# Performance work log

Measured on AMD Instinct MI355X. Metric: run time of the kernel, lower is better.

## Reference

```python
import jax, jax.numpy as jnp
import numpy as np

NPOINT = 1024
NSAMPLE = 32
BN_EPS = 1e-5


def setup_inputs() -> dict:
    key = jax.random.key(0)
    ks = jax.random.split(key, 8)
    B, N, C = 16, 4096, 64
    chans = [C + 3, 64, 64, 128]
    d = {
        "xyz": jax.random.normal(ks[0], (B, N, 3), jnp.float32),
        "points": jax.random.normal(ks[1], (B, N, C), jnp.float32),
    }
    for i in range(3):
        d[f"w{i+1}"] = jax.random.normal(ks[2 + i], (chans[i + 1], chans[i]), jnp.float32) / np.sqrt(chans[i]).astype(np.float32)
        d[f"b{i+1}"] = jnp.zeros((chans[i + 1],), jnp.float32)
        d[f"g{i+1}"] = jnp.ones((chans[i + 1],), jnp.float32)
        d[f"be{i+1}"] = jnp.zeros((chans[i + 1],), jnp.float32)
    return d


def farthest_point_sample(xyz, npoint):
    # xyz: [B, N, 3] -> centroids: [B, npoint] int32 (deterministic start at index 0)
    B, N, _ = xyz.shape

    def step(carry, _):
        distance, farthest = carry
        centroid = jnp.take_along_axis(xyz, farthest[:, None, None], axis=1)  # [B,1,3]
        dist = jnp.sum((xyz - centroid) ** 2, axis=-1)                         # [B,N]
        distance = jnp.minimum(distance, dist)
        new_far = jnp.argmax(distance, axis=-1).astype(jnp.int32)
        return (distance, new_far), farthest

    init = (jnp.full((B, N), 1e10, xyz.dtype), jnp.zeros((B,), jnp.int32))
    _, cents = jax.lax.scan(step, init, None, length=npoint)  # [npoint, B]
    return cents.T  # [B, npoint]


def index_points(points, idx):
    # points: [B,N,C], idx: [B,...] -> [B,...,C]
    return jax.vmap(lambda p, i: p[i])(points, idx)


def bn_relu(h, g, be):
    # training-mode BatchNorm over all axes except channel (last), biased var
    m = h.mean(axis=(0, 1, 2), keepdims=True)
    v = h.var(axis=(0, 1, 2), keepdims=True)
    return jax.nn.relu((h - m) / jnp.sqrt(v + BN_EPS) * g + be)


def reference(xyz, points, w1, b1, g1, be1, w2, b2, g2, be2, w3, b3, g3, be3):
    # --- sample_and_group ---
    fps_idx = farthest_point_sample(xyz, NPOINT)           # [B,S]
    new_xyz = index_points(xyz, fps_idx)                   # [B,S,3]
    # query_ball_point in source ignores radius: kNN via argsort of sq dists
    sqrdists = jnp.sum((new_xyz[:, :, None, :] - xyz[:, None, :, :]) ** 2, axis=-1)  # [B,S,N]
    _, group_idx = jax.lax.top_k(-sqrdists, NSAMPLE)       # [B,S,K] smallest distances
    grouped_xyz = index_points(xyz, group_idx) - new_xyz[:, :, None, :]  # [B,S,K,3]
    grouped_pts = index_points(points, group_idx)          # [B,S,K,C]
    new_points = jnp.concatenate([grouped_xyz, grouped_pts], axis=-1)    # [B,S,K,C+3]
    # --- shared MLP (1x1 conv + BN + ReLU) x3, channel-last layout ---
    h = bn_relu(jnp.einsum("bskc,oc->bsko", new_points, w1) + b1, g1, be1)
    h = bn_relu(jnp.einsum("bskc,oc->bsko", h, w2) + b2, g2, be2)
    h = bn_relu(jnp.einsum("bskc,oc->bsko", h, w3) + b3, g3, be3)
    # max-pool over the neighbor (nsample) axis
    out = jnp.max(h, axis=2)  # [B,S,128]
    return (new_xyz, out)
```

## Files before the change

### kernel.cpp

```cpp
#include <hip/hip_runtime.h>
#include <cstdint>

#define NB   16
#define NPT  4096
#define CINP 64
#define SP   1024
#define KNB  32
#define NROWS (NB*SP*KNB)
#define NT_F  524288.0f
#define NBLK  8192

__device__ __forceinline__ float sqdist3(float ax, float ay, float az,
                                         float bx, float by, float bz) {
  float dx = ax - bx, dy = ay - by, dz = az - bz;
  return __fadd_rn(__fadd_rn(__fmul_rn(dx, dx), __fmul_rn(dy, dy)), __fmul_rn(dz, dz));
}

__global__ __launch_bounds__(512) void fps_kernel(const float* __restrict__ xyz,
                                                  float* __restrict__ newxyz) {
  const int b = blockIdx.x, t = threadIdx.x;
  __shared__ float s_xyz[NPT * 3];
  __shared__ unsigned long long s_red[2][8];
  for (int i = t; i < NPT * 3; i += 512) s_xyz[i] = xyz[b * NPT * 3 + i];
  __syncthreads();
  float px[8], py[8], pz[8], dst[8];
#pragma unroll
  for (int j = 0; j < 8; ++j) {
    int p = t + j * 512;
    px[j] = s_xyz[p * 3 + 0];
    py[j] = s_xyz[p * 3 + 1];
    pz[j] = s_xyz[p * 3 + 2];
    dst[j] = 1e10f;
  }
  float cx = s_xyz[0], cy = s_xyz[1], cz = s_xyz[2];
  const int w = t >> 6, lane = t & 63;
  int buf = 0;
  for (int it = 0; it < SP; ++it) {
    if (t == 0) {
      float* o = newxyz + (b * SP + it) * 3;
      o[0] = cx; o[1] = cy; o[2] = cz;
    }
    unsigned long long best = 0;
#pragma unroll
    for (int j = 0; j < 8; ++j) {
      float d = sqdist3(px[j], py[j], pz[j], cx, cy, cz);
      dst[j] = fminf(dst[j], d);
      unsigned long long key =
          ((unsigned long long)__float_as_uint(dst[j]) << 32) |
          (unsigned)(4095 - (t + j * 512));
      best = key > best ? key : best;
    }
#pragma unroll
    for (int off = 32; off >= 1; off >>= 1) {
      unsigned long long o2 = __shfl_down(best, off);
      best = o2 > best ? o2 : best;
    }
    if (lane == 0) s_red[buf][w] = best;
    __syncthreads();
    unsigned long long k = s_red[buf][0];
#pragma unroll
    for (int i = 1; i < 8; ++i) {
      unsigned long long v = s_red[buf][i];
      k = v > k ? v : k;
    }
    int p = 4095 - (int)(k & 0xFFFFFFFFull);
    cx = s_xyz[p * 3 + 0];
    cy = s_xyz[p * 3 + 1];
    cz = s_xyz[p * 3 + 2];
    buf ^= 1;
  }
}

__global__ __launch_bounds__(256) void knn_kernel(const float* __restrict__ xyz,
                                                  const float* __restrict__ newxyz,
                                                  int* __restrict__ gidx) {
  const int t = threadIdx.x, lane = t & 63, w = t >> 6;
  const int q = blockIdx.x * 4 + w;
  const int b = q >> 10;
  const float* nx = newxyz + q * 3;
  const float qx = nx[0], qy = nx[1], qz = nx[2];
  const float* xb = xyz + b * NPT * 3;
  float d[64];
#pragma unroll
  for (int j = 0; j < 64; ++j) {
    int p = j * 64 + lane;
    d[j] = sqdist3(xb[p * 3], xb[p * 3 + 1], xb[p * 3 + 2], qx, qy, qz);
  }
  unsigned V = 0;
  for (int bit = 30; bit >= 0; --bit) {
    unsigned cand = V | (1u << bit);
    int c = 0;
#pragma unroll
    for (int j = 0; j < 64; ++j) c += (__float_as_uint(d[j]) < cand) ? 1 : 0;
#pragma unroll
    for (int off = 32; off >= 1; off >>= 1) c += __shfl_xor(c, off);
    if (c < KNB) V = cand;
  }
  __shared__ int s_cnt[4], s_eqcnt[4], s_eq[4][64];
  if (lane == 0) { s_cnt[w] = 0; s_eqcnt[w] = 0; }
  __syncthreads();
  int* gout = gidx + q * KNB;
#pragma unroll
  for (int j = 0; j < 64; ++j) {
    unsigned db = __float_as_uint(d[j]);
    if (db < V) {
      int pos = atomicAdd(&s_cnt[w], 1);
      if (pos < KNB) gout[pos] = j * 64 + lane;
    } else if (db == V) {
      int pos = atomicAdd(&s_eqcnt[w], 1);
      if (pos < 64) s_eq[w][pos] = j * 64 + lane;
    }
  }
  __syncthreads();
  if (lane == 0) {
    int c1 = s_cnt[w]; if (c1 > KNB) c1 = KNB;
    int ne = s_eqcnt[w]; if (ne > 64) ne = 64;
    int need = KNB - c1;
    for (int m = 0; m < need; ++m) {
      int bi = -1, bv = 0x7fffffff;
      for (int e = 0; e < ne; ++e) {
        int v = s_eq[w][e];
        if (v < bv) { bv = v; bi = e; }
      }
      gout[c1 + m] = bv;
      if (bi >= 0) s_eq[w][bi] = 0x7fffffff;
    }
  }
}

__global__ __launch_bounds__(256) void layer1_kernel(
    const float* __restrict__ xyz, const float* __restrict__ points,
    const float* __restrict__ newxyz, const int* __restrict__ gidx,
    const float* __restrict__ w1, const float* __restrict__ b1,
    float* __restrict__ h1, float* __restrict__ part) {
  const int t = threadIdx.x, blk = blockIdx.x;
  const int R0 = blk * 64;
  const int b = R0 >> 15;
  __shared__ __align__(16) float xs[67][68];
  __shared__ __align__(16) float wsm[67][68];
  __shared__ float red[2][16][64];
  {
    int o = t & 63;
    for (int c = t >> 6; c < 67; c += 4) wsm[c][o] = w1[o * 67 + c];
  }
  {
    int r = t >> 2, q = t & 3;
    int R = R0 + r;
    int idx = gidx[R];
    if (q == 0) {
      const float* xp = xyz + (size_t)(b * NPT + idx) * 3;
      const float* nq = newxyz + (size_t)(R >> 5) * 3;
      xs[0][r] = xp[0] - nq[0];
      xs[1][r] = xp[1] - nq[1];
      xs[2][r] = xp[2] - nq[2];
    }
    const float* pp = points + (size_t)(b * NPT + idx) * CINP + q * 16;
#pragma unroll
    for (int i = 0; i < 4; ++i) {
      float4 v = *(const float4*)(pp + i * 4);
      int c = 3 + q * 16 + i * 4;
      xs[c][r] = v.x; xs[c + 1][r] = v.y; xs[c + 2][r] = v.z; xs[c + 3][r] = v.w;
    }
  }
  __syncthreads();
  const int tr = t & 15, to = t >> 4;
  float acc[4][4];
#pragma unroll
  for (int j = 0; j < 4; ++j) {
    float bb = b1[to * 4 + j];
    acc[0][j] = bb; acc[1][j] = bb; acc[2][j] = bb; acc[3][j] = bb;
  }
  for (int c = 0; c < 67; ++c) {
    float4 xv = *(const float4*)&xs[c][tr * 4];
    float4 wv = *(const float4*)&wsm[c][to * 4];
    float xa[4] = {xv.x, xv.y, xv.z, xv.w};
    float wa[4] = {wv.x, wv.y, wv.z, wv.w};
#pragma unroll
    for (int i = 0; i < 4; ++i)
#pragma unroll
      for (int j = 0; j < 4; ++j) acc[i][j] += xa[i] * wa[j];
  }
#pragma unroll
  for (int i = 0; i < 4; ++i) {
    float4 st; st.x = acc[i][0]; st.y = acc[i][1]; st.z = acc[i][2]; st.w = acc[i][3];
    *(float4*)&h1[(size_t)(R0 + tr * 4 + i) * 64 + to * 4] = st;
  }
#pragma unroll
  for (int j = 0; j < 4; ++j) {
    float s1 = acc[0][j] + acc[1][j] + acc[2][j] + acc[3][j];
    float s2 = acc[0][j] * acc[0][j] + acc[1][j] * acc[1][j] +
               acc[2][j] * acc[2][j] + acc[3][j] * acc[3][j];
    red[0][tr][to * 4 + j] = s1;
    red[1][tr][to * 4 + j] = s2;
  }
  __syncthreads();
  if (t < 128) {
    int stat = t >> 6, o = t & 63;
    float v = 0.f;
#pragma unroll
    for (int k = 0; k < 16; ++k) v += red[stat][k][o];
    part[(size_t)(stat * 64 + o) * NBLK + blk] = v;
  }
}

__global__ __launch_bounds__(256) void layer2_kernel(
    const float* __restrict__ hin, const float* __restrict__ bn,
    const float* __restrict__ w2, const float* __restrict__ b2,
    float* __restrict__ hout, float* __restrict__ part) {
  const int t = threadIdx.x, blk = blockIdx.x;
  const size_t R0 = (size_t)blk * 64;
  __shared__ __align__(16) float xs[64][68];
  __shared__ __align__(16) float wsm[64][68];
  __shared__ float red[2][16][64];
  {
    int o = t & 63;
    for (int c = t >> 6; c < 64; c += 4) wsm[c][o] = w2[o * 64 + c];
  }
  {
    int r = t >> 2, q = t & 3;
    const float* hp = hin + (R0 + r) * 64 + q * 16;
#pragma unroll
    for (int i = 0; i < 4; ++i) {
      int c = q * 16 + i * 4;
      float4 v = *(const float4*)(hp + i * 4);
      float4 sc = *(const float4*)(bn + c);
      float4 sh = *(const float4*)(bn + 64 + c);
      xs[c][r]     = fmaxf(v.x * sc.x + sh.x, 0.f);
      xs[c + 1][r] = fmaxf(v.y * sc.y + sh.y, 0.f);
      xs[c + 2][r] = fmaxf(v.z * sc.z + sh.z, 0.f);
      xs[c + 3][r] = fmaxf(v.w * sc.w + sh.w, 0.f);
    }
  }
  __syncthreads();
  const int tr = t & 15, to = t >> 4;
  float acc[4][4];
#pragma unroll
  for (int j = 0; j < 4; ++j) {
    float bb = b2[to * 4 + j];
    acc[0][j] = bb; acc[1][j] = bb; acc[2][j] = bb; acc[3][j] = bb;
  }
  for (int c = 0; c < 64; ++c) {
    float4 xv = *(const float4*)&xs[c][tr * 4];
    float4 wv = *(const float4*)&wsm[c][to * 4];
    float xa[4] = {xv.x, xv.y, xv.z, xv.w};
    float wa[4] = {wv.x, wv.y, wv.z, wv.w};
#pragma unroll
    for (int i = 0; i < 4; ++i)
#pragma unroll
      for (int j = 0; j < 4; ++j) acc[i][j] += xa[i] * wa[j];
  }
#pragma unroll
  for (int i = 0; i < 4; ++i) {
    float4 st; st.x = acc[i][0]; st.y = acc[i][1]; st.z = acc[i][2]; st.w = acc[i][3];
    *(float4*)&hout[(R0 + tr * 4 + i) * 64 + to * 4] = st;
  }
#pragma unroll
  for (int j = 0; j < 4; ++j) {
    float s1 = acc[0][j] + acc[1][j] + acc[2][j] + acc[3][j];
    float s2 = acc[0][j] * acc[0][j] + acc[1][j] * acc[1][j] +
               acc[2][j] * acc[2][j] + acc[3][j] * acc[3][j];
    red[0][tr][to * 4 + j] = s1;
    red[1][tr][to * 4 + j] = s2;
  }
  __syncthreads();
  if (t < 128) {
    int stat = t >> 6, o = t & 63;
    float v = 0.f;
#pragma unroll
    for (int k = 0; k < 16; ++k) v += red[stat][k][o];
    part[(size_t)(stat * 64 + o) * NBLK + blk] = v;
  }
}

__global__ __launch_bounds__(256) void layer3_kernel(
    const float* __restrict__ hin, const float* __restrict__ bn,
    const float* __restrict__ w3, const float* __restrict__ b3,
    float* __restrict__ maxh, float* __restrict__ minh, float* __restrict__ part) {
  const int t = threadIdx.x, blk = blockIdx.x;
  const size_t R0 = (size_t)blk * 64;
  __shared__ __align__(16) float smem[64 * 68 + 64 * 136];
  float* xs = smem;
  float* wsm = smem + 64 * 68;
  {
    int o = t & 127, q = t >> 7;
    for (int c = q; c < 64; c += 2) wsm[c * 136 + o] = w3[o * 64 + c];
  }
  {
    int r = t >> 2, q = t & 3;
    const float* hp = hin + (R0 + r) * 64 + q * 16;
#pragma unroll
    for (int i = 0; i < 4; ++i) {
      int c = q * 16 + i * 4;
      float4 v = *(const float4*)(hp + i * 4);
      float4 sc = *(const float4*)(bn + c);
      float4 sh = *(const float4*)(bn + 64 + c);
      xs[c * 68 + r]       = fmaxf(v.x * sc.x + sh.x, 0.f);
      xs[(c + 1) * 68 + r] = fmaxf(v.y * sc.y + sh.y, 0.f);
      xs[(c + 2) * 68 + r] = fmaxf(v.z * sc.z + sh.z, 0.f);
      xs[(c + 3) * 68 + r] = fmaxf(v.w * sc.w + sh.w, 0.f);
    }
  }
  __syncthreads();
  const int tr = t & 15, to = t >> 4;
  float acc[4][8];
#pragma unroll
  for (int j = 0; j < 8; ++j) {
    float bb = b3[to * 8 + j];
#pragma unroll
    for (int i = 0; i < 4; ++i) acc[i][j] = bb;
  }
  for (int c = 0; c < 64; ++c) {
    float4 xv = *(const float4*)&xs[c * 68 + tr * 4];
    float4 wv0 = *(const float4*)&wsm[c * 136 + to * 8];
    float4 wv1 = *(const float4*)&wsm[c * 136 + to * 8 + 4];
    float xa[4] = {xv.x, xv.y, xv.z, xv.w};
    float wa[8] = {wv0.x, wv0.y, wv0.z, wv0.w, wv1.x, wv1.y, wv1.z, wv1.w};
#pragma unroll
    for (int i = 0; i < 4; ++i)
#pragma unroll
      for (int j = 0; j < 8; ++j) acc[i][j] += xa[i] * wa[j];
  }
  __syncthreads();
  float* red = smem;
#pragma unroll
  for (int j = 0; j < 8; ++j) {
    float s1 = acc[0][j] + acc[1][j] + acc[2][j] + acc[3][j];
    float s2 = acc[0][j] * acc[0][j] + acc[1][j] * acc[1][j] +
               acc[2][j] * acc[2][j] + acc[3][j] * acc[3][j];
    red[(0 * 16 + tr) * 128 + to * 8 + j] = s1;
    red[(1 * 16 + tr) * 128 + to * 8 + j] = s2;
  }
  __syncthreads();
  {
    int stat = t >> 7, o = t & 127;
    float v = 0.f;
#pragma unroll
    for (int k = 0; k < 16; ++k) v += red[(stat * 16 + k) * 128 + o];
    part[(size_t)(stat * 128 + o) * NBLK + blk] = v;
  }
  __syncthreads();
#pragma unroll
  for (int j = 0; j < 8; ++j) {
    float mx = fmaxf(fmaxf(acc[0][j], acc[1][j]), fmaxf(acc[2][j], acc[3][j]));
    float mn = fminf(fminf(acc[0][j], acc[1][j]), fminf(acc[2][j], acc[3][j]));
    red[(0 * 16 + tr) * 128 + to * 8 + j] = mx;
    red[(1 * 16 + tr) * 128 + to * 8 + j] = mn;
  }
  __syncthreads();
  {
    int g = t >> 7, o = t & 127;
    float mx = -1e30f, mn = 1e30f;
#pragma unroll
    for (int k = 0; k < 8; ++k) {
      mx = fmaxf(mx, red[(0 * 16 + g * 8 + k) * 128 + o]);
      mn = fminf(mn, red[(1 * 16 + g * 8 + k) * 128 + o]);
    }
    size_t bs = (size_t)blk * 2 + g;
    maxh[bs * 128 + o] = mx;
    minh[bs * 128 + o] = mn;
  }
}

__global__ __launch_bounds__(256) void bn_finalize(const float* __restrict__ part,
                                                   const float* __restrict__ g,
                                                   const float* __restrict__ be,
                                                   float* __restrict__ bnout, int Cout) {
  const int o = blockIdx.x, t = threadIdx.x;
  float s1 = 0.f, s2 = 0.f;
  const float* p1 = part + (size_t)o * NBLK;
  const float* p2 = part + (size_t)(Cout + o) * NBLK;
  for (int i = t; i < NBLK; i += 256) { s1 += p1[i]; s2 += p2[i]; }
#pragma unroll
  for (int off = 32; off >= 1; off >>= 1) {
    s1 += __shfl_xor(s1, off);
    s2 += __shfl_xor(s2, off);
  }
  __shared__ float r1[4], r2[4];
  if ((t & 63) == 0) { r1[t >> 6] = s1; r2[t >> 6] = s2; }
  __syncthreads();
  if (t == 0) {
    float S1 = r1[0] + r1[1] + r1[2] + r1[3];
    float S2 = r2[0] + r2[1] + r2[2] + r2[3];
    float m = S1 / NT_F;
    float v = S2 / NT_F - m * m;
    if (v < 0.f) v = 0.f;
    float inv = 1.0f / sqrtf(v + 1e-5f);
    float sc = g[o] * inv;
    bnout[o] = sc;
    bnout[Cout + o] = be[o] - m * sc;
  }
}

__global__ __launch_bounds__(256) void finalize_kernel(const float* __restrict__ maxh,
                                                       const float* __restrict__ minh,
                                                       const float* __restrict__ bn,
                                                       float* __restrict__ out2) {
  int i = blockIdx.x * 256 + threadIdx.x;
  int o = i & 127;
  float sc = bn[o], sh = bn[128 + o];
  float a = sc * maxh[i] + sh;
  float c = sc * minh[i] + sh;
  out2[i] = fmaxf(fmaxf(a, c), 0.f);
}

extern "C" void kernel_launch(void* const* d_in, const int* in_sizes, int n_in,
                              void* d_out, int out_size, void* d_ws, size_t ws_size,
                              hipStream_t stream) {
  const float* xyz = (const float*)d_in[0];
  const float* points = (const float*)d_in[1];
  const float* w1 = (const float*)d_in[2];
  const float* b1 = (const float*)d_in[3];
  const float* g1 = (const float*)d_in[4];
  const float* be1 = (const float*)d_in[5];
  const float* w2 = (const float*)d_in[6];
  const float* b2 = (const float*)d_in[7];
  const float* g2 = (const float*)d_in[8];
  const float* be2 = (const float*)d_in[9];
  const float* w3 = (const float*)d_in[10];
  const float* b3 = (const float*)d_in[11];
  const float* g3 = (const float*)d_in[12];
  const float* be3 = (const float*)d_in[13];

  float* out = (float*)d_out;
  float* newxyz = out;
  float* out2 = out + 49152;

  const size_t MiB = 1u << 20;
  char* wsb = (char*)d_ws;
  int*   gidx = (int*)wsb;
  float* h    = (float*)(wsb + 2 * MiB);
  float* part = (float*)(wsb + 130 * MiB);
  float* maxh = (float*)(wsb + 138 * MiB);
  float* minh = (float*)(wsb + 146 * MiB);
  float* bn1  = (float*)(wsb + 154 * MiB);
  float* bn2  = bn1 + 128;
  float* bn3  = bn2 + 128;

  hipLaunchKernelGGL(fps_kernel, dim3(NB), dim3(512), 0, stream, xyz, newxyz);
  hipLaunchKernelGGL(knn_kernel, dim3(16384 / 4), dim3(256), 0, stream, xyz, newxyz, gidx);
  hipLaunchKernelGGL(layer1_kernel, dim3(NBLK), dim3(256), 0, stream,
                     xyz, points, newxyz, gidx, w1, b1, h, part);
  hipLaunchKernelGGL(bn_finalize, dim3(64), dim3(256), 0, stream, part, g1, be1, bn1, 64);
  hipLaunchKernelGGL(layer2_kernel, dim3(NBLK), dim3(256), 0, stream, h, bn1, w2, b2, h, part);
  hipLaunchKernelGGL(bn_finalize, dim3(64), dim3(256), 0, stream, part, g2, be2, bn2, 64);
  hipLaunchKernelGGL(layer3_kernel, dim3(NBLK), dim3(256), 0, stream,
                     h, bn2, w3, b3, maxh, minh, part);
  hipLaunchKernelGGL(bn_finalize, dim3(128), dim3(256), 0, stream, part, g3, be3, bn3, 128);
  hipLaunchKernelGGL(finalize_kernel, dim3(2097152 / 256), dim3(256), 0, stream,
                     maxh, minh, bn3, out2);
}
```

Measured before the change: 1.468 ms.

## Rework FPS with packed-float DPP reductions and enlarge layer1/2 row tiles

The FPS kernel now runs 256 threads per batch, stores points padded to float4 in LDS, computes distances with 2-wide packed float vectors, and replaces the 64-bit shuffle reduction with DPP max/min reductions on float distance and index. The kNN radix-select count reduction also moves to a DPP sum. Layers 1 and 2 process 128 rows per block with a 4x8 register tile, which halves the block count and the BN partial-sum count. The intent is to shorten the serial per-iteration latency of the FPS loop, which dominates the runtime. In exchange the FPS kernel has fewer waves per batch, and the matmul kernels use more registers per thread.

```diff
diff --git a/kernel.cpp b/kernel.cpp
--- a/kernel.cpp
+++ b/kernel.cpp
@@ -8,7 +8,10 @@
 #define KNB  32
 #define NROWS (NB*SP*KNB)
 #define NT_F  524288.0f
-#define NBLK  8192
+#define NBLK12 4096
+#define NBLK3  8192
+
+typedef float v2f __attribute__((ext_vector_type(2)));
 
 __device__ __forceinline__ float sqdist3(float ax, float ay, float az,
                                          float bx, float by, float bz) {
@@ -16,57 +19,112 @@
   return __fadd_rn(__fadd_rn(__fmul_rn(dx, dx), __fmul_rn(dy, dy)), __fmul_rn(dz, dz));
 }
 
-__global__ __launch_bounds__(512) void fps_kernel(const float* __restrict__ xyz,
+#define DPP_STAGE_MAXF(v, ctrl)                                                   \
+  do {                                                                            \
+    int _t = __builtin_amdgcn_update_dpp(0, __float_as_int(v), ctrl, 0xf, 0xf, false); \
+    v = fmaxf(v, __int_as_float(_t));                                             \
+  } while (0)
+
+__device__ __forceinline__ float wave_max_f32(float v) {
+  DPP_STAGE_MAXF(v, 0x111);
+  DPP_STAGE_MAXF(v, 0x112);
+  DPP_STAGE_MAXF(v, 0x114);
+  DPP_STAGE_MAXF(v, 0x118);
+  DPP_STAGE_MAXF(v, 0x142);
+  DPP_STAGE_MAXF(v, 0x143);
+  return __int_as_float(__builtin_amdgcn_readlane(__float_as_int(v), 63));
+}
+
+#define DPP_STAGE_MINU(v, ctrl)                                                   \
+  do {                                                                            \
+    unsigned _t = (unsigned)__builtin_amdgcn_update_dpp(                          \
+        (int)0xFFFFFFFF, (int)(v), ctrl, 0xf, 0xf, false);                        \
+    v = (v < _t) ? v : _t;                                                        \
+  } while (0)
+
+__device__ __forceinline__ unsigned wave_min_u32(unsigned v) {
+  DPP_STAGE_MINU(v, 0x111);
+  DPP_STAGE_MINU(v, 0x112);
+  DPP_STAGE_MINU(v, 0x114);
+  DPP_STAGE_MINU(v, 0x118);
+  DPP_STAGE_MINU(v, 0x142);
+  DPP_STAGE_MINU(v, 0x143);
+  return (unsigned)__builtin_amdgcn_readlane((int)v, 63);
+}
+
+#define DPP_STAGE_ADDI(v, ctrl)                                                   \
+  do {                                                                            \
+    int _t = __builtin_amdgcn_update_dpp(0, (v), ctrl, 0xf, 0xf, false);          \
+    v += _t;                                                                      \
+  } while (0)
+
+__device__ __forceinline__ int wave_sum_i32(int v) {
+  DPP_STAGE_ADDI(v, 0x111);
+  DPP_STAGE_ADDI(v, 0x112);
+  DPP_STAGE_ADDI(v, 0x114);
+  DPP_STAGE_ADDI(v, 0x118);
+  DPP_STAGE_ADDI(v, 0x142);
+  DPP_STAGE_ADDI(v, 0x143);
+  return __builtin_amdgcn_readlane(v, 63);
+}
+
+__global__ __launch_bounds__(256) void fps_kernel(const float* __restrict__ xyz,
                                                   float* __restrict__ newxyz) {
+#pragma clang fp contract(off)
   const int b = blockIdx.x, t = threadIdx.x;
-  __shared__ float s_xyz[NPT * 3];
-  __shared__ unsigned long long s_red[2][8];
-  for (int i = t; i < NPT * 3; i += 512) s_xyz[i] = xyz[b * NPT * 3 + i];
-  __syncthreads();
-  float px[8], py[8], pz[8], dst[8];
-#pragma unroll
-  for (int j = 0; j < 8; ++j) {
-    int p = t + j * 512;
-    px[j] = s_xyz[p * 3 + 0];
-    py[j] = s_xyz[p * 3 + 1];
-    pz[j] = s_xyz[p * 3 + 2];
-    dst[j] = 1e10f;
-  }
-  float cx = s_xyz[0], cy = s_xyz[1], cz = s_xyz[2];
-  const int w = t >> 6, lane = t & 63;
+  __shared__ __align__(16) float s4[NPT * 4];
+  __shared__ unsigned long long s_red[2][4];
+  const float* gx = xyz + b * NPT * 3;
+  for (int i = t; i < NPT * 3; i += 256) s4[(i / 3) * 4 + (i % 3)] = gx[i];
+  __syncthreads();
+  v2f px[8], py[8], pz[8], dst[8];
+#pragma unroll
+  for (int k = 0; k < 8; ++k) {
+    float4 a = *(const float4*)&s4[(t + (2 * k) * 256) * 4];
+    float4 c = *(const float4*)&s4[(t + (2 * k + 1) * 256) * 4];
+    px[k].x = a.x; px[k].y = c.x;
+    py[k].x = a.y; py[k].y = c.y;
+    pz[k].x = a.z; pz[k].y = c.z;
+    dst[k].x = 1e10f; dst[k].y = 1e10f;
+  }
+  float cx = s4[0], cy = s4[1], cz = s4[2];
+  const int w = t >> 6;
   int buf = 0;
   for (int it = 0; it < SP; ++it) {
     if (t == 0) {
       float* o = newxyz + (b * SP + it) * 3;
       o[0] = cx; o[1] = cy; o[2] = cz;
     }
-    unsigned long long best = 0;
-#pragma unroll
-    for (int j = 0; j < 8; ++j) {
-      float d = sqdist3(px[j], py[j], pz[j], cx, cy, cz);
-      dst[j] = fminf(dst[j], d);
-      unsigned long long key =
-          ((unsigned long long)__float_as_uint(dst[j]) << 32) |
-          (unsigned)(4095 - (t + j * 512));
-      best = key > best ? key : best;
-    }
-#pragma unroll
-    for (int off = 32; off >= 1; off >>= 1) {
-      unsigned long long o2 = __shfl_down(best, off);
-      best = o2 > best ? o2 : best;
-    }
-    if (lane == 0) s_red[buf][w] = best;
+    v2f vcx; vcx.x = cx; vcx.y = cx;
+    v2f vcy; vcy.x = cy; vcy.y = cy;
+    v2f vcz; vcz.x = cz; vcz.y = cz;
+    float bd = -1.0f; int bi = 0;
+#pragma unroll
+    for (int k = 0; k < 8; ++k) {
+      v2f dx = px[k] - vcx;
+      v2f dy = py[k] - vcy;
+      v2f dz = pz[k] - vcz;
+      v2f dd = (dx * dx + dy * dy) + dz * dz;
+      float n0 = fminf(dst[k].x, dd.x);
+      float n1 = fminf(dst[k].y, dd.y);
+      dst[k].x = n0; dst[k].y = n1;
+      if (n0 > bd) { bd = n0; bi = t + (2 * k) * 256; }
+      if (n1 > bd) { bd = n1; bi = t + (2 * k + 1) * 256; }
+    }
+    float dw = wave_max_f32(bd);
+    unsigned cand = (bd == dw) ? (unsigned)bi : 0xFFFFFFFFu;
+    unsigned iw = wave_min_u32(cand);
+    if ((t & 63) == 0)
+      s_red[buf][w] = ((unsigned long long)__float_as_uint(dw) << 32) | (4095u - iw);
     __syncthreads();
-    unsigned long long k = s_red[buf][0];
-#pragma unroll
-    for (int i = 1; i < 8; ++i) {
-      unsigned long long v = s_red[buf][i];
-      k = v > k ? v : k;
-    }
-    int p = 4095 - (int)(k & 0xFFFFFFFFull);
-    cx = s_xyz[p * 3 + 0];
-    cy = s_xyz[p * 3 + 1];
-    cz = s_xyz[p * 3 + 2];
+    unsigned long long k0 = s_red[buf][0], k1 = s_red[buf][1];
+    unsigned long long k2 = s_red[buf][2], k3 = s_red[buf][3];
+    unsigned long long ka = k0 > k1 ? k0 : k1;
+    unsigned long long kb = k2 > k3 ? k2 : k3;
+    unsigned long long km = ka > kb ? ka : kb;
+    int p = 4095 - (int)(km & 0xFFFFFFFFull);
+    float4 cc = *(const float4*)&s4[p * 4];
+    cx = cc.x; cy = cc.y; cz = cc.z;
     buf ^= 1;
   }
 }
@@ -92,9 +150,8 @@
     int c = 0;
 #pragma unroll
     for (int j = 0; j < 64; ++j) c += (__float_as_uint(d[j]) < cand) ? 1 : 0;
-#pragma unroll
-    for (int off = 32; off >= 1; off >>= 1) c += __shfl_xor(c, off);
-    if (c < KNB) V = cand;
+    int ct = wave_sum_i32(c);
+    if (ct < KNB) V = cand;
   }
   __shared__ int s_cnt[4], s_eqcnt[4], s_eq[4][64];
   if (lane == 0) { s_cnt[w] = 0; s_eqcnt[w] = 0; }
@@ -134,17 +191,17 @@
     const float* __restrict__ w1, const float* __restrict__ b1,
     float* __restrict__ h1, float* __restrict__ part) {
   const int t = threadIdx.x, blk = blockIdx.x;
-  const int R0 = blk * 64;
+  const int R0 = blk * 128;
   const int b = R0 >> 15;
-  __shared__ __align__(16) float xs[67][68];
+  __shared__ __align__(16) float xs[67][132];
   __shared__ __align__(16) float wsm[67][68];
-  __shared__ float red[2][16][64];
+  __shared__ float red[2][32][64];
   {
     int o = t & 63;
     for (int c = t >> 6; c < 67; c += 4) wsm[c][o] = w1[o * 67 + c];
   }
   {
-    int r = t >> 2, q = t & 3;
+    int r = t >> 1, q = t & 1;
     int R = R0 + r;
     int idx = gidx[R];
     if (q == 0) {
@@ -154,52 +211,57 @@
       xs[1][r] = xp[1] - nq[1];
       xs[2][r] = xp[2] - nq[2];
     }
-    const float* pp = points + (size_t)(b * NPT + idx) * CINP + q * 16;
-#pragma unroll
-    for (int i = 0; i < 4; ++i) {
+    const float* pp = points + (size_t)(b * NPT + idx) * CINP + q * 32;
+#pragma unroll
+    for (int i = 0; i < 8; ++i) {
       float4 v = *(const float4*)(pp + i * 4);
-      int c = 3 + q * 16 + i * 4;
+      int c = 3 + q * 32 + i * 4;
       xs[c][r] = v.x; xs[c + 1][r] = v.y; xs[c + 2][r] = v.z; xs[c + 3][r] = v.w;
     }
   }
   __syncthreads();
-  const int tr = t & 15, to = t >> 4;
-  float acc[4][4];
-#pragma unroll
-  for (int j = 0; j < 4; ++j) {
-    float bb = b1[to * 4 + j];
-    acc[0][j] = bb; acc[1][j] = bb; acc[2][j] = bb; acc[3][j] = bb;
+  const int tr = t & 31, to = t >> 5;
+  float acc[4][8];
+#pragma unroll
+  for (int j = 0; j < 8; ++j) {
+    float bb = b1[to * 8 + j];
+#pragma unroll
+    for (int i = 0; i < 4; ++i) acc[i][j] = bb;
   }
   for (int c = 0; c < 67; ++c) {
     float4 xv = *(const float4*)&xs[c][tr * 4];
-    float4 wv = *(const float4*)&wsm[c][to * 4];
+    float4 w0 = *(const float4*)&wsm[c][to * 8];
+    float4 w1v = *(const float4*)&wsm[c][to * 8 + 4];
     float xa[4] = {xv.x, xv.y, xv.z, xv.w};
-    float wa[4] = {wv.x, wv.y, wv.z, wv.w};
+    float wa[8] = {w0.x, w0.y, w0.z, w0.w, w1v.x, w1v.y, w1v.z, w1v.w};
 #pragma unroll
     for (int i = 0; i < 4; ++i)
 #pragma unroll
-      for (int j = 0; j < 4; ++j) acc[i][j] += xa[i] * wa[j];
+      for (int j = 0; j < 8; ++j) acc[i][j] += xa[i] * wa[j];
   }
 #pragma unroll
   for (int i = 0; i < 4; ++i) {
-    float4 st; st.x = acc[i][0]; st.y = acc[i][1]; st.z = acc[i][2]; st.w = acc[i][3];
-    *(float4*)&h1[(size_t)(R0 + tr * 4 + i) * 64 + to * 4] = st;
-  }
-#pragma unroll
-  for (int j = 0; j < 4; ++j) {
+    float4 s0; s0.x = acc[i][0]; s0.y = acc[i][1]; s0.z = acc[i][2]; s0.w = acc[i][3];
+    float4 s1; s1.x = acc[i][4]; s1.y = acc[i][5]; s1.z = acc[i][6]; s1.w = acc[i][7];
+    float* hp = &h1[(size_t)(R0 + tr * 4 + i) * 64 + to * 8];
+    *(float4*)hp = s0;
+    *(float4*)(hp + 4) = s1;
+  }
+#pragma unroll
+  for (int j = 0; j < 8; ++j) {
     float s1 = acc[0][j] + acc[1][j] + acc[2][j] + acc[3][j];
     float s2 = acc[0][j] * acc[0][j] + acc[1][j] * acc[1][j] +
                acc[2][j] * acc[2][j] + acc[3][j] * acc[3][j];
-    red[0][tr][to * 4 + j] = s1;
-    red[1][tr][to * 4 + j] = s2;
+    red[0][tr][to * 8 + j] = s1;
+    red[1][tr][to * 8 + j] = s2;
   }
   __syncthreads();
   if (t < 128) {
     int stat = t >> 6, o = t & 63;
     float v = 0.f;
 #pragma unroll
-    for (int k = 0; k < 16; ++k) v += red[stat][k][o];
-    part[(size_t)(stat * 64 + o) * NBLK + blk] = v;
+    for (int k = 0; k < 32; ++k) v += red[stat][k][o];
+    part[(size_t)(stat * 64 + o) * NBLK12 + blk] = v;
   }
 }
 
@@ -208,20 +270,20 @@
     const float* __restrict__ w2, const float* __restrict__ b2,
     float* __restrict__ hout, float* __restrict__ part) {
   const int t = threadIdx.x, blk = blockIdx.x;
-  const size_t R0 = (size_t)blk * 64;
-  __shared__ __align__(16) float xs[64][68];
+  const size_t R0 = (size_t)blk * 128;
+  __shared__ __align__(16) float xs[64][132];
   __shared__ __align__(16) float wsm[64][68];
-  __shared__ float red[2][16][64];
+  __shared__ float red[2][32][64];
   {
     int o = t & 63;
     for (int c = t >> 6; c < 64; c += 4) wsm[c][o] = w2[o * 64 + c];
   }
   {
-    int r = t >> 2, q = t & 3;
-    const float* hp = hin + (R0 + r) * 64 + q * 16;
-#pragma unroll
-    for (int i = 0; i < 4; ++i) {
-      int c = q * 16 + i * 4;
+    int r = t >> 1, q = t & 1;
+    const float* hp = hin + (R0 + r) * 64 + q * 32;
+#pragma unroll
+    for (int i = 0; i < 8; ++i) {
+      int c = q * 32 + i * 4;
       float4 v = *(const float4*)(hp + i * 4);
       float4 sc = *(const float4*)(bn + c);
       float4 sh = *(const float4*)(bn + 64 + c);
@@ -232,43 +294,48 @@
     }
   }
   __syncthreads();
-  const int tr = t & 15, to = t >> 4;
-  float acc[4][4];
-#pragma unroll
-  for (int j = 0; j < 4; ++j) {
-    float bb = b2[to * 4 + j];
-    acc[0][j] = bb; acc[1][j] = bb; acc[2][j] = bb; acc[3][j] = bb;
+  const int tr = t & 31, to = t >> 5;
+  float acc[4][8];
+#pragma unroll
+  for (int j = 0; j < 8; ++j) {
+    float bb = b2[to * 8 + j];
+#pragma unroll
+    for (int i = 0; i < 4; ++i) acc[i][j] = bb;
   }
   for (int c = 0; c < 64; ++c) {
     float4 xv = *(const float4*)&xs[c][tr * 4];
-    float4 wv = *(const float4*)&wsm[c][to * 4];
+    float4 w0 = *(const float4*)&wsm[c][to * 8];
+    float4 w1v = *(const float4*)&wsm[c][to * 8 + 4];
     float xa[4] = {xv.x, xv.y, xv.z, xv.w};
-    float wa[4] = {wv.x, wv.y, wv.z, wv.w};
+    float wa[8] = {w0.x, w0.y, w0.z, w0.w, w1v.x, w1v.y, w1v.z, w1v.w};
 #pragma unroll
     for (int i = 0; i < 4; ++i)
 #pragma unroll
-      for (int j = 0; j < 4; ++j) acc[i][j] += xa[i] * wa[j];
+      for (int j = 0; j < 8; ++j) acc[i][j] += xa[i] * wa[j];
   }
 #pragma unroll
   for (int i = 0; i < 4; ++i) {
-    float4 st; st.x = acc[i][0]; st.y = acc[i][1]; st.z = acc[i][2]; st.w = acc[i][3];
-    *(float4*)&hout[(R0 + tr * 4 + i) * 64 + to * 4] = st;
-  }
-#pragma unroll
-  for (int j = 0; j < 4; ++j) {
+    float4 s0; s0.x = acc[i][0]; s0.y = acc[i][1]; s0.z = acc[i][2]; s0.w = acc[i][3];
+    float4 s1; s1.x = acc[i][4]; s1.y = acc[i][5]; s1.z = acc[i][6]; s1.w = acc[i][7];
+    float* hp = &hout[(R0 + tr * 4 + i) * 64 + to * 8];
+    *(float4*)hp = s0;
+    *(float4*)(hp + 4) = s1;
+  }
+#pragma unroll
+  for (int j = 0; j < 8; ++j) {
     float s1 = acc[0][j] + acc[1][j] + acc[2][j] + acc[3][j];
     float s2 = acc[0][j] * acc[0][j] + acc[1][j] * acc[1][j] +
                acc[2][j] * acc[2][j] + acc[3][j] * acc[3][j];
-    red[0][tr][to * 4 + j] = s1;
-    red[1][tr][to * 4 + j] = s2;
+    red[0][tr][to * 8 + j] = s1;
+    red[1][tr][to * 8 + j] = s2;
   }
   __syncthreads();
   if (t < 128) {
     int stat = t >> 6, o = t & 63;
     float v = 0.f;
 #pragma unroll
-    for (int k = 0; k < 16; ++k) v += red[stat][k][o];
-    part[(size_t)(stat * 64 + o) * NBLK + blk] = v;
+    for (int k = 0; k < 32; ++k) v += red[stat][k][o];
+    part[(size_t)(stat * 64 + o) * NBLK12 + blk] = v;
   }
 }
 
@@ -336,7 +403,7 @@
     float v = 0.f;
 #pragma unroll
     for (int k = 0; k < 16; ++k) v += red[(stat * 16 + k) * 128 + o];
-    part[(size_t)(stat * 128 + o) * NBLK + blk] = v;
+    part[(size_t)(stat * 128 + o) * NBLK3 + blk] = v;
   }
   __syncthreads();
 #pragma unroll
@@ -364,12 +431,13 @@
 __global__ __launch_bounds__(256) void bn_finalize(const float* __restrict__ part,
                                                    const float* __restrict__ g,
                                                    const float* __restrict__ be,
-                                                   float* __restrict__ bnout, int Cout) {
+                                                   float* __restrict__ bnout,
+                                                   int Cout, int nblk) {
   const int o = blockIdx.x, t = threadIdx.x;
   float s1 = 0.f, s2 = 0.f;
-  const float* p1 = part + (size_t)o * NBLK;
-  const float* p2 = part + (size_t)(Cout + o) * NBLK;
-  for (int i = t; i < NBLK; i += 256) { s1 += p1[i]; s2 += p2[i]; }
+  const float* p1 = part + (size_t)o * nblk;
+  const float* p2 = part + (size_t)(Cout + o) * nblk;
+  for (int i = t; i < nblk; i += 256) { s1 += p1[i]; s2 += p2[i]; }
 #pragma unroll
   for (int off = 32; off >= 1; off >>= 1) {
     s1 += __shfl_xor(s1, off);
@@ -436,16 +504,16 @@
   float* bn2  = bn1 + 128;
   float* bn3  = bn2 + 128;
 
-  hipLaunchKernelGGL(fps_kernel, dim3(NB), dim3(512), 0, stream, xyz, newxyz);
+  hipLaunchKernelGGL(fps_kernel, dim3(NB), dim3(256), 0, stream, xyz, newxyz);
   hipLaunchKernelGGL(knn_kernel, dim3(16384 / 4), dim3(256), 0, stream, xyz, newxyz, gidx);
-  hipLaunchKernelGGL(layer1_kernel, dim3(NBLK), dim3(256), 0, stream,
+  hipLaunchKernelGGL(layer1_kernel, dim3(NBLK12), dim3(256), 0, stream,
                      xyz, points, newxyz, gidx, w1, b1, h, part);
-  hipLaunchKernelGGL(bn_finalize, dim3(64), dim3(256), 0, stream, part, g1, be1, bn1, 64);
-  hipLaunchKernelGGL(layer2_kernel, dim3(NBLK), dim3(256), 0, stream, h, bn1, w2, b2, h, part);
-  hipLaunchKernelGGL(bn_finalize, dim3(64), dim3(256), 0, stream, part, g2, be2, bn2, 64);
-  hipLaunchKernelGGL(layer3_kernel, dim3(NBLK), dim3(256), 0, stream,
+  hipLaunchKernelGGL(bn_finalize, dim3(64), dim3(256), 0, stream, part, g1, be1, bn1, 64, NBLK12);
+  hipLaunchKernelGGL(layer2_kernel, dim3(NBLK12), dim3(256), 0, stream, h, bn1, w2, b2, h, part);
+  hipLaunchKernelGGL(bn_finalize, dim3(64), dim3(256), 0, stream, part, g2, be2, bn2, 64, NBLK12);
+  hipLaunchKernelGGL(layer3_kernel, dim3(NBLK3), dim3(256), 0, stream,
                      h, bn2, w3, b3, maxh, minh, part);
-  hipLaunchKernelGGL(bn_finalize, dim3(128), dim3(256), 0, stream, part, g3, be3, bn3, 128);
+  hipLaunchKernelGGL(bn_finalize, dim3(128), dim3(256), 0, stream, part, g3, be3, bn3, 128, NBLK3);
   hipLaunchKernelGGL(finalize_kernel, dim3(2097152 / 256), dim3(256), 0, stream,
                      maxh, minh, bn3, out2);
 }
```

Result: faster. 1.336 ms (-8.9%).
